# Performance work log

Hardware: AMD Instinct MI355X
Metric: run time of the kernel (lower is better)

Reference implementation:

```python
import jax, jax.numpy as jnp
import numpy as np

CUTOFF = 4.0
D_RBF = 20


def _rbf_consts():
    # e3nn soft_one_hot_linspace, basis='gaussian', cutoff=False
    values = np.linspace(0.0, CUTOFF, D_RBF)
    step = values[1] - values[0]
    # RadialBasis normalization buffers: 4000 uniform samples, unbiased std
    rs = np.linspace(0.0, CUTOFF, 4001)[1:]
    bs = np.exp(-(((rs[:, None] - values[None, :]) / step) ** 2)) / 1.12
    mean = bs.mean(0)
    inv_std = 1.0 / bs.std(0, ddof=1)
    return (jnp.asarray(values, jnp.float32), jnp.float32(step),
            jnp.asarray(mean, jnp.float32), jnp.asarray(inv_std, jnp.float32))


def setup_inputs() -> dict:
    N, P, E = 2000, 50000, 300000
    Ds, Dv, H, HO = 256, 128, 256, 128
    din = Ds + Dv + D_RBF + Dv  # 532
    key = jax.random.key(0)
    ks = jax.random.split(key, 12)
    atom_xyz = jax.random.uniform(ks[0], (N, 3), jnp.float32, 0.0, 8.0)
    probe_xyz = jax.random.uniform(ks[1], (P, 3), jnp.float32, 0.0, 8.0)
    cell = jnp.eye(3, dtype=jnp.float32)[None] * 8.0  # [1,3,3]
    src = jax.random.randint(ks[2], (E,), 0, N)
    dst = jax.random.randint(ks[3], (E,), 0, P)
    edges = jnp.stack([src, dst], axis=-1).astype(jnp.int32)  # [E,2]
    edges_displacement = jax.random.randint(ks[4], (E, 3), -1, 2).astype(jnp.float32)
    S_final = jax.random.normal(ks[5], (N, Ds), jnp.float32)
    V_final = jax.random.normal(ks[6], (N, Dv, 3), jnp.float32)
    s = 0.02
    return {
        'atom_xyz': atom_xyz, 'probe_xyz': probe_xyz, 'cell': cell,
        'edges': edges, 'edges_displacement': edges_displacement,
        'S_final': S_final, 'V_final': V_final,
        'ln_gamma': jnp.ones((din,), jnp.float32),
        'ln_beta': jnp.zeros((din,), jnp.float32),
        'W1': jax.random.normal(ks[7], (din, H), jnp.float32) * s,
        'b1': jnp.zeros((H,), jnp.float32),
        'W2': jax.random.normal(ks[8], (H, H), jnp.float32) * s,
        'b2': jnp.zeros((H,), jnp.float32),
        'Wo1': jax.random.normal(ks[9], (H, HO), jnp.float32) * s,
        'bo1': jnp.zeros((HO,), jnp.float32),
        'Wo2': jax.random.normal(ks[10], (HO, 1), jnp.float32) * s,
        'bo2': jnp.full((1,), -10.0, jnp.float32),
    }


def reference(atom_xyz, probe_xyz, cell, edges, edges_displacement,
              S_final, V_final, ln_gamma, ln_beta,
              W1, b1, W2, b2, Wo1, bo1, Wo2, bo2):
    values, step, rbf_mean, rbf_inv_std = _rbf_consts()
    src, dst = edges[:, 0], edges[:, 1]
    # PBC displacement: edges_displacement @ cell (single graph -> cell[0])
    disp = edges_displacement @ cell[0]                     # [E,3]
    vec = probe_xyz[dst] - (atom_xyz[src] + disp)           # [E,3]
    d = jnp.maximum(jnp.linalg.norm(vec, axis=-1, keepdims=True), 1e-8)
    r_hat = vec / d                                         # [E,3]
    ds = d[:, 0]                                            # [E]
    # RBF (gaussian soft one-hot) + normalization
    diff = (ds[:, None] - values) / step
    e = (jnp.exp(-diff * diff) / 1.12 - rbf_mean) * rbf_inv_std  # [E,20]
    x = ds / CUTOFF
    x5 = x ** 5
    env = (1.0 - 21.0 * x5 + 35.0 * x5 * x - 15.0 * x5 * x * x)
    env = env * (ds < CUTOFF).astype(jnp.float32)           # [E]
    # geometric invariants
    q = jnp.einsum('ek,eck->ec', r_hat, V_final[src])       # [E,Dv]
    n_atom = jnp.linalg.norm(V_final, axis=-1)              # [N,Dv]
    feat = jnp.concatenate([S_final[src], n_atom[src], e, q], axis=-1)  # [E,532]
    # LayerNorm
    mu = feat.mean(-1, keepdims=True)
    var = feat.var(-1, keepdims=True)
    feat = (feat - mu) * jax.lax.rsqrt(var + 1e-5) * ln_gamma + ln_beta
    # message MLP
    h = jax.nn.silu(feat @ W1 + b1)
    h = jax.nn.silu(h @ W2 + b2)                            # [E,256]
    # envelope-weighted scatter-add to probes
    m_p = jax.ops.segment_sum(h * env[:, None], dst,
                              num_segments=probe_xyz.shape[0])  # [P,256]
    # output MLP
    o = jax.nn.silu(m_p @ Wo1 + bo1)
    rho = o @ Wo2 + bo2                                     # [P,1]
    return rho[:, 0]
```

## Files before the change

### kernel.cpp

```cpp
#include <hip/hip_runtime.h>
#include <hip/hip_bf16.h>
#include <hip/hip_fp16.h>

#define DIN 532
#define DRBF 20
#define EB 32

typedef __attribute__((ext_vector_type(8))) short s8v;
typedef __attribute__((ext_vector_type(4))) float f4v;

static __device__ __forceinline__ float silu_f(float x){
    return x * __builtin_amdgcn_rcpf(1.0f + __expf(-x));
}
static __device__ __forceinline__ short f2bf(float x){
    __hip_bfloat16 b = __float2bfloat16(x);
    return *(short*)&b;
}
static __device__ __forceinline__ s8v pack8(float4 f0, float4 f1){
    s8v r;
    r[0]=f2bf(f0.x); r[1]=f2bf(f0.y); r[2]=f2bf(f0.z); r[3]=f2bf(f0.w);
    r[4]=f2bf(f1.x); r[5]=f2bf(f1.y); r[6]=f2bf(f1.z); r[7]=f2bf(f1.w);
    return r;
}
static __device__ __forceinline__ s8v pack8p(const float* p){
    float4 f0 = *(const float4*)p, f1 = *(const float4*)(p + 4);
    return pack8(f0, f1);
}
static __device__ __forceinline__ bool detect_bf16(const void* cellraw){
    float c0 = ((const float*)cellraw)[0];
    return !(c0 > 7.5f && c0 < 8.5f);
}
static __device__ __forceinline__ float loadr(const void* p, bool isbf, long idx){
    if (isbf) return __bfloat162float(((const __hip_bfloat16*)p)[idx]);
    return ((const float*)p)[idx];
}

struct ConvArgs {
    const void* src[9];
    float*      dst[9];
    int         sz[9];
    int         total;
    const void* cell;
};

__global__ void k_convert(ConvArgs a){
    bool isbf = detect_bf16(a.cell);
    int stride = gridDim.x * blockDim.x;
    for (int i = blockIdx.x*blockDim.x + threadIdx.x; i < a.total; i += stride){
        int idx = i, k = 0;
        while (idx >= a.sz[k]) { idx -= a.sz[k]; k++; }
        float v;
        if (isbf) v = __bfloat162float(((const __hip_bfloat16*)a.src[k])[idx]);
        else      v = ((const float*)a.src[k])[idx];
        a.dst[k][idx] = v;
    }
}

__global__ __launch_bounds__(256) void k_prep(
    const void* W1r, const void* gammar, const void* betar, const void* b1r,
    const void* W2r, const void* Wo1r, const void* cellraw,
    float* Gv, float* Bb, float* rbfc,
    short* w1ef, short* w2f, short* w1f, short* wo1f)
{
    int b = blockIdx.x, t = threadIdx.x;
    bool isbf = detect_bf16(cellraw);
    if (b < 17){
        int i0 = b * 32, i1 = min(i0 + 32, DIN);
        float g = 0.0f, bb = 0.0f;
        for (int i = i0; i < i1; i++){
            float w  = loadr(W1r, isbf, (long)i*256 + t);
            g  += loadr(gammar, isbf, i) * w;
            bb += loadr(betar,  isbf, i) * w;
        }
        if (b == 0) bb += loadr(b1r, isbf, t);
        atomicAdd(&Gv[t], g);
        atomicAdd(&Bb[t], bb);
        return;
    }
    if (b == 17){
        __shared__ float ssum[DRBF][8], ssq[DRBF][8];
        if (t < 160){
            int m = t >> 3, c = t & 7;
            const float step = 4.0f/19.0f;
            float vm = step * m;
            float s = 0.0f, ss = 0.0f;
            for (int i = c*500 + 1; i <= c*500 + 500; i++){
                float r = 0.001f * (float)i;
                float u = (r - vm) / step;
                float bv = __expf(-u*u) * (1.0f/1.12f);
                s += bv; ss += bv*bv;
            }
            ssum[m][c] = s; ssq[m][c] = ss;
        }
        __syncthreads();
        if (t < DRBF){
            float s = 0.0f, ss = 0.0f;
            for (int c = 0; c < 8; c++){ s += ssum[t][c]; ss += ssq[t][c]; }
            float mean = s / 4000.0f;
            float var  = (ss - s*s/4000.0f) / 3999.0f;
            rbfc[t]        = mean;
            rbfc[DRBF + t] = rsqrtf(var);
        }
        return;
    }
    int wid = t >> 6, lane = t & 63;
    int q8 = (lane >> 4) * 8, nl = lane & 15;
    if (b <= 21){
        int f = (b - 18)*4 + wid;
        for (int j = 0; j < 8; j++){
            int kk = q8 + j;
            int n  = f*16 + nl;
            float v = (kk < DRBF)
                ? loadr(gammar, isbf, 384 + kk) * loadr(W1r, isbf, (long)(384 + kk)*256 + n)
                : 0.0f;
            w1ef[((f << 6) | lane)*8 + j] = f2bf(v);
        }
    } else if (b <= 53){
        int f = (b - 22)*4 + wid;
        int ks = f & 7;
        for (int j = 0; j < 8; j++){
            int kk = ks*32 + q8 + j;
            int n  = (f >> 3)*16 + nl;
            w2f[((f << 6) | lane)*8 + j] = f2bf(loadr(W2r, isbf, (long)kk*256 + n));
        }
    } else if (b <= 117){
        int f = (b - 54)*4 + wid;
        int ksg = f >> 4, ntg = f & 15;
        int base;
        if (ksg < 8)       base = ksg * 32;
        else if (ksg < 12) base = 256 + (ksg - 8) * 32;
        else               base = 404 + (ksg - 12) * 32;
        for (int j = 0; j < 8; j++){
            int kk = base + q8 + j;
            int n  = ntg*16 + nl;
            w1f[((f << 6) | lane)*8 + j] =
                f2bf(loadr(gammar, isbf, kk) * loadr(W1r, isbf, (long)kk*256 + n));
        }
    } else {
        int f = (b - 118)*4 + wid;
        int ks = f & 7;
        for (int j = 0; j < 8; j++){
            int kk = ks*32 + q8 + j;
            int n  = (f >> 3)*16 + nl;
            wo1f[((f << 6) | lane)*8 + j] = f2bf(loadr(Wo1r, isbf, (long)kk*128 + n));
        }
    }
}

__global__ __launch_bounds__(256) void k_atom(const float* S, const float* V,
                                              const short* w1f, float4* AM,
                                              float* scal, int N){
    __shared__ float Sl[16][260];
    __shared__ float Vxl[16][132], Vyl[16][132], Vzl[16][132], nll[16][132];
    int t = threadIdx.x, wid = t >> 6, lane = t & 63;
    int q = lane >> 4, ml = lane & 15;
    int a0 = blockIdx.x * 16;

    for (int a = 0; a < 16; a++){
        int atom = min(a0 + a, N - 1);
        Sl[a][t] = S[atom*256 + t];
        if (t < 128){
            float x = V[atom*384 + 3*t];
            float y = V[atom*384 + 3*t + 1];
            float z = V[atom*384 + 3*t + 2];
            Vxl[a][t] = x; Vyl[a][t] = y; Vzl[a][t] = z;
            nll[a][t] = sqrtf(x*x + y*y + z*z);
        }
    }
    __syncthreads();

    for (int a2 = 0; a2 < 4; a2++){
        int a = (wid << 2) + a2;
        float v[11];
        #pragma unroll
        for (int k = 0; k < 11; k++) v[k] = 0.0f;
        for (int e = lane; e < 256; e += 64){
            float s = Sl[a][e];
            v[0] += s; v[1] += s*s;
        }
        for (int e = lane; e < 128; e += 64){
            float n = nll[a][e], x = Vxl[a][e], y = Vyl[a][e], z = Vzl[a][e];
            v[0] += n;   v[1] += n*n;
            v[2] += x;   v[3] += y;   v[4] += z;
            v[5] += x*x; v[6] += x*y; v[7] += x*z;
            v[8] += y*y; v[9] += y*z; v[10] += z*z;
        }
        #pragma unroll
        for (int k = 0; k < 11; k++)
            for (int off = 32; off > 0; off >>= 1)
                v[k] += __shfl_xor(v[k], off, 64);
        if (lane == 0 && a0 + a < N)
            for (int k = 0; k < 11; k++) scal[(a0 + a)*12 + k] = v[k];
    }

    f4v zz = {0.0f, 0.0f, 0.0f, 0.0f};
    f4v aA1[4], aM0[4], aM1[4], aM2[4];
    #pragma unroll
    for (int nt = 0; nt < 4; nt++){ aA1[nt]=zz; aM0[nt]=zz; aM1[nt]=zz; aM2[nt]=zz; }

    #pragma unroll
    for (int ks = 0; ks < 8; ks++){
        s8v av = pack8p(&Sl[ml][ks*32 + q*8]);
        #pragma unroll
        for (int nt = 0; nt < 4; nt++){
            s8v b = ((const s8v*)w1f)[(((ks << 4) | ((wid << 2) | nt)) << 6) | lane];
            aA1[nt] = __builtin_amdgcn_mfma_f32_16x16x32_bf16(av, b, aA1[nt], 0, 0, 0);
        }
    }
    #pragma unroll
    for (int ks = 0; ks < 4; ks++){
        s8v av = pack8p(&nll[ml][ks*32 + q*8]);
        #pragma unroll
        for (int nt = 0; nt < 4; nt++){
            s8v b = ((const s8v*)w1f)[((((8 + ks) << 4) | ((wid << 2) | nt)) << 6) | lane];
            aA1[nt] = __builtin_amdgcn_mfma_f32_16x16x32_bf16(av, b, aA1[nt], 0, 0, 0);
        }
    }
    #pragma unroll
    for (int ks = 0; ks < 4; ks++){
        s8v ax = pack8p(&Vxl[ml][ks*32 + q*8]);
        s8v ay = pack8p(&Vyl[ml][ks*32 + q*8]);
        s8v az = pack8p(&Vzl[ml][ks*32 + q*8]);
        #pragma unroll
        for (int nt = 0; nt < 4; nt++){
            s8v b = ((const s8v*)w1f)[((((12 + ks) << 4) | ((wid << 2) | nt)) << 6) | lane];
            aM0[nt] = __builtin_amdgcn_mfma_f32_16x16x32_bf16(ax, b, aM0[nt], 0, 0, 0);
            aM1[nt] = __builtin_amdgcn_mfma_f32_16x16x32_bf16(ay, b, aM1[nt], 0, 0, 0);
            aM2[nt] = __builtin_amdgcn_mfma_f32_16x16x32_bf16(az, b, aM2[nt], 0, 0, 0);
        }
    }

    #pragma unroll
    for (int nt = 0; nt < 4; nt++){
        #pragma unroll
        for (int reg = 0; reg < 4; reg++){
            int atom = a0 + (q << 2) + reg;
            if (atom < N)
                AM[(size_t)atom*256 + ((wid << 6) | (nt << 4) | ml)] =
                    make_float4(aA1[nt][reg], aM0[nt][reg], aM1[nt][reg], aM2[nt][reg]);
        }
    }
}

__global__ __launch_bounds__(256) void k_geom(
    const int* edges, const void* edraw, const float* cell,
    const float* axyz, const float* pxyz,
    int* etot, int* flag, int2* esd, float4* geo,
    const void* cellraw, int E)
{
    __shared__ int wcnt[4], wbase[4];
    bool isbf = detect_bf16(cellraw);
    float c0=cell[0],c1=cell[1],c2=cell[2],c3=cell[3],c4=cell[4];
    float c5=cell[5],c6=cell[6],c7=cell[7],c8=cell[8];
    int t = threadIdx.x, wid = t >> 6, lane = t & 63;
    int i = blockIdx.x*256 + t;

    bool act = false;
    int s = 0, dd = 0;
    float r0 = 0.f, r1 = 0.f, r2 = 0.f, dn = 0.f;
    if (i < E){
        s = edges[2*i]; dd = edges[2*i + 1];
        float d0 = loadr(edraw, isbf, 3L*i);
        float d1 = loadr(edraw, isbf, 3L*i + 1);
        float d2 = loadr(edraw, isbf, 3L*i + 2);
        float dx = d0*c0 + d1*c3 + d2*c6;
        float dy = d0*c1 + d1*c4 + d2*c7;
        float dz = d0*c2 + d1*c5 + d2*c8;
        float vx = pxyz[3*dd]   - (axyz[3*s]   + dx);
        float vy = pxyz[3*dd+1] - (axyz[3*s+1] + dy);
        float vz = pxyz[3*dd+2] - (axyz[3*s+2] + dz);
        dn = fmaxf(sqrtf(vx*vx + vy*vy + vz*vz), 1e-8f);
        act = dn < 4.0f;
        float inv = __builtin_amdgcn_rcpf(dn);
        r0 = vx*inv; r1 = vy*inv; r2 = vz*inv;
    }
    unsigned long long mask = __ballot(act);
    if (lane == 0) wcnt[wid] = __popcll(mask);
    __syncthreads();
    if (t == 0){
        int tot = wcnt[0] + wcnt[1] + wcnt[2] + wcnt[3];
        int base = tot ? atomicAdd(etot, tot) : 0;
        int run = base;
        #pragma unroll
        for (int w2 = 0; w2 < 4; w2++){ wbase[w2] = run; run += wcnt[w2]; }
    }
    __syncthreads();
    if (act){
        int pos = wbase[wid] + __popcll(mask & ((1ULL << lane) - 1ULL));
        esd[pos] = make_int2(s, dd);
        geo[pos] = make_float4(r0, r1, r2, dn);
        flag[dd] = 1;
    }
}

__global__ void k_zero(const int* flag, float4* m_p4, int P){
    int gid = blockIdx.x*256 + threadIdx.x;
    int row = gid >> 2, seg = gid & 3;
    if (row < P && flag[row]){
        float4 z = make_float4(0.f, 0.f, 0.f, 0.f);
        float4* p = m_p4 + (size_t)row*64 + seg*16;
        #pragma unroll
        for (int i = 0; i < 16; i++) p[i] = z;
    }
}

__global__ __launch_bounds__(256, 2) void k_edge(
    const int2* esd, const float4* geo, const int* etot, const float* scal,
    const float4* AM, const float* Gv, const float* Bb, const float* b2,
    const short* w1ef, const short* w2f, const float* rbfc, float* m_p)
{
    __shared__ float Gl[256], Bbl[256], b2l[256];
    __shared__ float rmean[DRBF], rinv[DRBF];
    __shared__ int   esrc[EB], edst[EB];
    __shared__ float rh0[EB], rh1[EB], rh2[EB], envv[EB], muv[EB], av[EB];
    __shared__ __align__(16) short ebfl[EB][32];
    __shared__ __align__(16) short afrag[2][8][64][8];

    int t = threadIdx.x, wid = t >> 6, lane = t & 63;
    int q = lane >> 4, ml_ = lane & 15;
    Gl[t] = Gv[t]; Bbl[t] = Bb[t]; b2l[t] = b2[t];
    if (t < DRBF){ rmean[t] = rbfc[t]; rinv[t] = rbfc[DRBF + t]; }
    __syncthreads();

    int Ea = etot[0];
    int ntiles = (Ea + EB - 1) / EB;

    for (int tile = blockIdx.x; tile < ntiles; tile += gridDim.x){
        if (t < EB){
            int epos = tile*EB + t;
            if (epos < Ea){
                int2 sd = esd[epos];
                float4 g = geo[epos];
                float r0 = g.x, r1 = g.y, r2 = g.z, dn = g.w;
                float x = dn * 0.25f;
                float x2 = x*x, x4 = x2*x2, x5 = x4*x;
                float env = 1.0f - 21.0f*x5 + 35.0f*x5*x - 15.0f*x5*x2;
                const float step = 4.0f/19.0f;
                float se = 0.0f, sse = 0.0f;
                for (int m = 0; m < DRBF; m++){
                    float u  = (dn - step*m) / step;
                    float bv = __expf(-u*u) * (1.0f/1.12f);
                    float em = (bv - rmean[m]) * rinv[m];
                    ebfl[t][m] = f2bf(em);
                    se += em; sse += em*em;
                }
                for (int m = DRBF; m < 32; m++) ebfl[t][m] = 0;
                const float* sc = &scal[sd.x*12];
                float sumq = r0*sc[2] + r1*sc[3] + r2*sc[4];
                float ssqq = r0*r0*sc[5] + r1*r1*sc[8] + r2*r2*sc[10]
                           + 2.0f*(r0*r1*sc[6] + r0*r2*sc[7] + r1*r2*sc[9]);
                float mu  = (sc[0] + se + sumq) * (1.0f/(float)DIN);
                float msq = (sc[1] + sse + ssqq) * (1.0f/(float)DIN);
                float a   = rsqrtf(fmaxf(msq - mu*mu, 0.0f) + 1e-5f);
                esrc[t] = sd.x; edst[t] = sd.y;
                rh0[t] = r0; rh1[t] = r1; rh2[t] = r2;
                envv[t] = env; muv[t] = mu; av[t] = a;
            } else {
                esrc[t] = 0; edst[t] = 0;
                rh0[t] = rh1[t] = rh2[t] = 0.0f;
                envv[t] = 0.0f; muv[t] = 0.0f; av[t] = 0.0f;
                for (int m = 0; m < 32; m++) ebfl[t][m] = 0;
            }
        }
        __syncthreads();

        f4v zz = {0.0f, 0.0f, 0.0f, 0.0f};
        f4v az[2][4];
        s8v ea0 = *(const s8v*)&ebfl[ml_][q*8];
        s8v ea1 = *(const s8v*)&ebfl[16 + ml_][q*8];
        #pragma unroll
        for (int nt = 0; nt < 4; nt++){
            s8v bw = ((const s8v*)w1ef)[(((wid << 2) | nt) << 6) | lane];
            az[0][nt] = __builtin_amdgcn_mfma_f32_16x16x32_bf16(ea0, bw, zz, 0, 0, 0);
            az[1][nt] = __builtin_amdgcn_mfma_f32_16x16x32_bf16(ea1, bw, zz, 0, 0, 0);
        }

        float gk[4], bbk[4];
        #pragma unroll
        for (int nt = 0; nt < 4; nt++){
            int k = (wid << 6) | (nt << 4) | ml_;
            gk[nt] = Gl[k]; bbk[nt] = Bbl[k];
        }
        #pragma unroll
        for (int mt = 0; mt < 2; mt++){
            #pragma unroll
            for (int reg = 0; reg < 4; reg++){
                int e_ = (mt << 4) | (q << 2) | reg;
                int s_ = esrc[e_];
                float r0 = rh0[e_], r1 = rh1[e_], r2 = rh2[e_];
                float mu = muv[e_], a_ = av[e_];
                const float4* AMr = &AM[(size_t)s_*256 + ((wid << 6) | ml_)];
                #pragma unroll
                for (int nt = 0; nt < 4; nt++){
                    float4 am = AMr[nt << 4];
                    float z = az[mt][nt][reg] + am.x + r0*am.y + r1*am.z + r2*am.w;
                    float y = a_*(z - mu*gk[nt]) + bbk[nt];
                    float h1 = silu_f(y);
                    int ks = (wid << 1) | (nt >> 1);
                    int col = ((nt & 1) << 4) | ml_;
                    int lanep = ((col >> 3) << 4) | (q << 2) | reg;
                    afrag[mt][ks][lanep][col & 7] = f2bf(h1);
                }
            }
        }
        __syncthreads();

        f4v acc[2][4];
        #pragma unroll
        for (int mt = 0; mt < 2; mt++)
            #pragma unroll
            for (int nt = 0; nt < 4; nt++) acc[mt][nt] = zz;
        #pragma unroll
        for (int ks = 0; ks < 8; ks++){
            s8v a0 = *(const s8v*)&afrag[0][ks][lane][0];
            s8v a1 = *(const s8v*)&afrag[1][ks][lane][0];
            #pragma unroll
            for (int nt = 0; nt < 4; nt++){
                s8v b = ((const s8v*)w2f)[(((((wid << 2) | nt) << 3) | ks) << 6) | lane];
                acc[0][nt] = __builtin_amdgcn_mfma_f32_16x16x32_bf16(a0, b, acc[0][nt], 0, 0, 0);
                acc[1][nt] = __builtin_amdgcn_mfma_f32_16x16x32_bf16(a1, b, acc[1][nt], 0, 0, 0);
            }
        }

        float b2k[4];
        #pragma unroll
        for (int nt = 0; nt < 4; nt++) b2k[nt] = b2l[(wid << 6) | (nt << 4) | ml_];
        #pragma unroll
        for (int mt = 0; mt < 2; mt++){
            #pragma unroll
            for (int reg = 0; reg < 4; reg++){
                int e_ = (mt << 4) | (q << 2) | reg;
                float env = envv[e_];
                if (env != 0.0f){
                    int dd = edst[e_];
                    float* mrow = &m_p[(size_t)dd*256 + (wid << 6) + ml_];
                    #pragma unroll
                    for (int nt = 0; nt < 4; nt++){
                        float z2 = acc[mt][nt][reg] + b2k[nt];
                        atomicAdd(&mrow[nt << 4], silu_f(z2) * env);
                    }
                }
            }
        }
        __syncthreads();
    }
}

__global__ __launch_bounds__(256) void k_probe(
    const float* m_p, const int* flag, const short* wo1f, const float* bo1,
    const float* Wo2, const float* bo2, void* out, const void* cellraw, int P)
{
    int t = threadIdx.x, wid = t >> 6, lane = t & 63;
    int q = lane >> 4, ml = lane & 15;
    int p0 = blockIdx.x * 128 + wid * 32;
    const float4* mp4 = (const float4*)m_p;

    f4v zz = {0.0f, 0.0f, 0.0f, 0.0f};
    f4v acc[2][8];
    #pragma unroll
    for (int mt = 0; mt < 2; mt++)
        #pragma unroll
        for (int nt = 0; nt < 8; nt++) acc[mt][nt] = zz;

    int row0 = min(p0 + ml, P - 1);
    int row1 = min(p0 + 16 + ml, P - 1);
    bool f0 = flag[row0] != 0;
    bool f1 = flag[row1] != 0;
    s8v zero8 = {0,0,0,0,0,0,0,0};

    #pragma unroll
    for (int ks = 0; ks < 8; ks++){
        int c = ks*8 + q*2;
        s8v a0 = zero8, a1 = zero8;
        if (f0){
            float4 f00 = mp4[(size_t)row0*64 + c], f01 = mp4[(size_t)row0*64 + c + 1];
            a0 = pack8(f00, f01);
        }
        if (f1){
            float4 f10 = mp4[(size_t)row1*64 + c], f11 = mp4[(size_t)row1*64 + c + 1];
            a1 = pack8(f10, f11);
        }
        #pragma unroll
        for (int nt = 0; nt < 8; nt++){
            s8v b = ((const s8v*)wo1f)[(((nt << 3) | ks) << 6) | lane];
            acc[0][nt] = __builtin_amdgcn_mfma_f32_16x16x32_bf16(a0, b, acc[0][nt], 0, 0, 0);
            acc[1][nt] = __builtin_amdgcn_mfma_f32_16x16x32_bf16(a1, b, acc[1][nt], 0, 0, 0);
        }
    }

    float bo1v[8], wo2v[8];
    #pragma unroll
    for (int nt = 0; nt < 8; nt++){
        int n = (nt << 4) | ml;
        bo1v[nt] = bo1[n];
        wo2v[nt] = Wo2[n];
    }
    bool isbf = detect_bf16(cellraw);
    float bo2v = bo2[0];

    #pragma unroll
    for (int mt = 0; mt < 2; mt++){
        #pragma unroll
        for (int reg = 0; reg < 4; reg++){
            float s = 0.0f;
            #pragma unroll
            for (int nt = 0; nt < 8; nt++)
                s += silu_f(acc[mt][nt][reg] + bo1v[nt]) * wo2v[nt];
            s += __shfl_xor(s, 1, 64);
            s += __shfl_xor(s, 2, 64);
            s += __shfl_xor(s, 4, 64);
            s += __shfl_xor(s, 8, 64);
            if (ml == 0){
                int p = p0 + (mt << 4) + (q << 2) + reg;
                if (p < P){
                    float rho = s + bo2v;
                    if (isbf) ((__hip_bfloat16*)out)[p] = __float2bfloat16(rho);
                    else      ((float*)out)[p] = rho;
                }
            }
        }
    }
}

extern "C" void kernel_launch(void* const* d_in, const int* in_sizes, int n_in,
                              void* d_out, int out_size, void* d_ws, size_t ws_size,
                              hipStream_t stream)
{
    const int N = in_sizes[0] / 3;
    const int P = in_sizes[1] / 3;
    const int E = in_sizes[3] / 2;

    float* w = (float*)d_ws;
    size_t off = 0;
    auto carve = [&](size_t n) -> float* {
        float* p = w + off;
        off += (n + 63) & ~(size_t)63;
        return p;
    };

    const int conv_din[9] = {6, 5, 1, 0, 12, 14, 15, 2, 16};
    float* cdst[9];
    int    csz[9];
    int total = 0;
    for (int k = 0; k < 9; k++){
        csz[k]  = in_sizes[conv_din[k]];
        cdst[k] = carve(csz[k]);
        total  += csz[k];
    }
    float* c_V     = cdst[0];
    float* c_S     = cdst[1];
    float* c_probe = cdst[2];
    float* c_atom  = cdst[3];
    float* c_b2    = cdst[4];
    float* c_bo1   = cdst[5];
    float* c_Wo2   = cdst[6];
    float* c_cell  = cdst[7];
    float* c_bo2   = cdst[8];

    float* rbfc  = carve(2 * DRBF);
    float* AMf   = carve((size_t)N * 256 * 4);
    float* scal  = carve((size_t)N * 12);
    float* w1ef  = carve(16 * 64 * 8 / 2);
    float* w2f   = carve(128 * 64 * 8 / 2);
    float* w1f   = carve(256 * 64 * 8 / 2);
    float* wo1f  = carve(64 * 64 * 8 / 2);
    float* m_p   = carve((size_t)P * 256);
    int*   etot  = (int*)carve(64);
    int*   flag  = (int*)carve(P);
    float* Gv    = carve(256);
    float* Bb    = carve(256);
    int*   esd   = (int*)carve((size_t)E * 2);
    float* geo   = carve((size_t)E * 4);

    ConvArgs ca;
    for (int k = 0; k < 9; k++){
        ca.src[k] = d_in[conv_din[k]];
        ca.dst[k] = cdst[k];
        ca.sz[k]  = csz[k];
    }
    ca.total = total;
    ca.cell  = d_in[2];

    const int* d_edges = (const int*)d_in[3];

    size_t zbytes = (size_t)((char*)(Bb + 256) - (char*)etot);
    hipMemsetAsync(etot, 0, zbytes, stream);
    k_convert<<<256, 256, 0, stream>>>(ca);
    k_prep<<<134, 256, 0, stream>>>(d_in[9], d_in[7], d_in[8], d_in[10],
                                    d_in[11], d_in[13], d_in[2],
                                    Gv, Bb, rbfc,
                                    (short*)w1ef, (short*)w2f, (short*)w1f, (short*)wo1f);
    k_atom<<<(N + 15) / 16, 256, 0, stream>>>(c_S, c_V, (const short*)w1f,
                                              (float4*)AMf, scal, N);
    k_geom<<<(E + 255) / 256, 256, 0, stream>>>(
        d_edges, d_in[4], c_cell, c_atom, c_probe,
        etot, flag, (int2*)esd, (float4*)geo, d_in[2], E);
    k_zero<<<(P*4 + 255) / 256, 256, 0, stream>>>(flag, (float4*)m_p, P);
    k_edge<<<512, 256, 0, stream>>>(
        (const int2*)esd, (const float4*)geo, etot, scal,
        (const float4*)AMf, Gv, Bb, c_b2,
        (const short*)w1ef, (const short*)w2f, rbfc, m_p);
    k_probe<<<(P + 127) / 128, 256, 0, stream>>>(
        m_p, flag, (const short*)wo1f, c_bo1, c_Wo2, c_bo2, d_out, d_in[2], P);
}
```

Before: 208.0 us.

## Merge small launches into fused pre and mid kernels, drop memset and zero kernel

Merges the convert and prep kernels into one launch, and the atom, geometry and Gv/Bb reduction into a single multi-role kernel. The memset is replaced by zeroing etot and flag inside the convert path, and m_p rows are now zeroed on first touch via atomicExch in the geometry blocks. Atomic accumulation of Gv/Bb is replaced by per-block partials reduced in the mid kernel. The aim is to cut launch overhead and the separate zero pass. In exchange, the atom path reads S directly from global memory instead of shared memory, and first-touch zeroing runs serially per row inside geometry threads.

```diff
diff --git a/kernel.cpp b/kernel.cpp
--- a/kernel.cpp
+++ b/kernel.cpp
@@ -36,48 +36,46 @@
 }
 
 struct ConvArgs {
-    const void* src[9];
-    float*      dst[9];
-    int         sz[9];
+    const void* src[10];
+    float*      dst[10];
+    int         sz[10];
     int         total;
-    const void* cell;
 };
 
-__global__ void k_convert(ConvArgs a){
-    bool isbf = detect_bf16(a.cell);
-    int stride = gridDim.x * blockDim.x;
-    for (int i = blockIdx.x*blockDim.x + threadIdx.x; i < a.total; i += stride){
-        int idx = i, k = 0;
-        while (idx >= a.sz[k]) { idx -= a.sz[k]; k++; }
-        float v;
-        if (isbf) v = __bfloat162float(((const __hip_bfloat16*)a.src[k])[idx]);
-        else      v = ((const float*)a.src[k])[idx];
-        a.dst[k][idx] = v;
-    }
-}
-
-__global__ __launch_bounds__(256) void k_prep(
+__global__ __launch_bounds__(256) void k_pre(ConvArgs ca,
     const void* W1r, const void* gammar, const void* betar, const void* b1r,
     const void* W2r, const void* Wo1r, const void* cellraw,
-    float* Gv, float* Bb, float* rbfc,
+    float* Gpart, float* Bpart, float* rbfc,
     short* w1ef, short* w2f, short* w1f, short* wo1f)
 {
     int b = blockIdx.x, t = threadIdx.x;
     bool isbf = detect_bf16(cellraw);
-    if (b < 17){
-        int i0 = b * 32, i1 = min(i0 + 32, DIN);
+    if (b < 256){
+        int stride = 256 * 256;
+        for (int i = b*256 + t; i < ca.total; i += stride){
+            int idx = i, k = 0;
+            while (idx >= ca.sz[k]) { idx -= ca.sz[k]; k++; }
+            float v = 0.0f;
+            if (ca.src[k]) v = loadr(ca.src[k], isbf, idx);
+            ca.dst[k][idx] = v;
+        }
+        return;
+    }
+    int pb = b - 256;
+    if (pb < 17){
+        int i0 = pb * 32, i1 = min(i0 + 32, DIN);
         float g = 0.0f, bb = 0.0f;
         for (int i = i0; i < i1; i++){
             float w  = loadr(W1r, isbf, (long)i*256 + t);
             g  += loadr(gammar, isbf, i) * w;
             bb += loadr(betar,  isbf, i) * w;
         }
-        if (b == 0) bb += loadr(b1r, isbf, t);
-        atomicAdd(&Gv[t], g);
-        atomicAdd(&Bb[t], bb);
+        if (pb == 0) bb += loadr(b1r, isbf, t);
+        Gpart[pb*256 + t] = g;
+        Bpart[pb*256 + t] = bb;
         return;
     }
-    if (b == 17){
+    if (pb == 17){
         __shared__ float ssum[DRBF][8], ssq[DRBF][8];
         if (t < 160){
             int m = t >> 3, c = t & 7;
@@ -105,8 +103,8 @@
     }
     int wid = t >> 6, lane = t & 63;
     int q8 = (lane >> 4) * 8, nl = lane & 15;
-    if (b <= 21){
-        int f = (b - 18)*4 + wid;
+    if (pb <= 21){
+        int f = (pb - 18)*4 + wid;
         for (int j = 0; j < 8; j++){
             int kk = q8 + j;
             int n  = f*16 + nl;
@@ -115,16 +113,16 @@
                 : 0.0f;
             w1ef[((f << 6) | lane)*8 + j] = f2bf(v);
         }
-    } else if (b <= 53){
-        int f = (b - 22)*4 + wid;
+    } else if (pb <= 53){
+        int f = (pb - 22)*4 + wid;
         int ks = f & 7;
         for (int j = 0; j < 8; j++){
             int kk = ks*32 + q8 + j;
             int n  = (f >> 3)*16 + nl;
             w2f[((f << 6) | lane)*8 + j] = f2bf(loadr(W2r, isbf, (long)kk*256 + n));
         }
-    } else if (b <= 117){
-        int f = (b - 54)*4 + wid;
+    } else if (pb <= 117){
+        int f = (pb - 54)*4 + wid;
         int ksg = f >> 4, ntg = f & 15;
         int base;
         if (ksg < 8)       base = ksg * 32;
@@ -137,7 +135,7 @@
                 f2bf(loadr(gammar, isbf, kk) * loadr(W1r, isbf, (long)kk*256 + n));
         }
     } else {
-        int f = (b - 118)*4 + wid;
+        int f = (pb - 118)*4 + wid;
         int ks = f & 7;
         for (int j = 0; j < 8; j++){
             int kk = ks*32 + q8 + j;
@@ -147,161 +145,171 @@
     }
 }
 
-__global__ __launch_bounds__(256) void k_atom(const float* S, const float* V,
-                                              const short* w1f, float4* AM,
-                                              float* scal, int N){
-    __shared__ float Sl[16][260];
-    __shared__ float Vxl[16][132], Vyl[16][132], Vzl[16][132], nll[16][132];
-    int t = threadIdx.x, wid = t >> 6, lane = t & 63;
-    int q = lane >> 4, ml = lane & 15;
-    int a0 = blockIdx.x * 16;
-
-    for (int a = 0; a < 16; a++){
-        int atom = min(a0 + a, N - 1);
-        Sl[a][t] = S[atom*256 + t];
-        if (t < 128){
-            float x = V[atom*384 + 3*t];
-            float y = V[atom*384 + 3*t + 1];
-            float z = V[atom*384 + 3*t + 2];
-            Vxl[a][t] = x; Vyl[a][t] = y; Vzl[a][t] = z;
-            nll[a][t] = sqrtf(x*x + y*y + z*z);
-        }
-    }
-    __syncthreads();
-
-    for (int a2 = 0; a2 < 4; a2++){
-        int a = (wid << 2) + a2;
-        float v[11];
-        #pragma unroll
-        for (int k = 0; k < 11; k++) v[k] = 0.0f;
-        for (int e = lane; e < 256; e += 64){
-            float s = Sl[a][e];
-            v[0] += s; v[1] += s*s;
-        }
-        for (int e = lane; e < 128; e += 64){
-            float n = nll[a][e], x = Vxl[a][e], y = Vyl[a][e], z = Vzl[a][e];
-            v[0] += n;   v[1] += n*n;
-            v[2] += x;   v[3] += y;   v[4] += z;
-            v[5] += x*x; v[6] += x*y; v[7] += x*z;
-            v[8] += y*y; v[9] += y*z; v[10] += z*z;
-        }
-        #pragma unroll
-        for (int k = 0; k < 11; k++)
-            for (int off = 32; off > 0; off >>= 1)
-                v[k] += __shfl_xor(v[k], off, 64);
-        if (lane == 0 && a0 + a < N)
-            for (int k = 0; k < 11; k++) scal[(a0 + a)*12 + k] = v[k];
-    }
-
-    f4v zz = {0.0f, 0.0f, 0.0f, 0.0f};
-    f4v aA1[4], aM0[4], aM1[4], aM2[4];
-    #pragma unroll
-    for (int nt = 0; nt < 4; nt++){ aA1[nt]=zz; aM0[nt]=zz; aM1[nt]=zz; aM2[nt]=zz; }
-
-    #pragma unroll
-    for (int ks = 0; ks < 8; ks++){
-        s8v av = pack8p(&Sl[ml][ks*32 + q*8]);
-        #pragma unroll
-        for (int nt = 0; nt < 4; nt++){
-            s8v b = ((const s8v*)w1f)[(((ks << 4) | ((wid << 2) | nt)) << 6) | lane];
-            aA1[nt] = __builtin_amdgcn_mfma_f32_16x16x32_bf16(av, b, aA1[nt], 0, 0, 0);
-        }
-    }
-    #pragma unroll
-    for (int ks = 0; ks < 4; ks++){
-        s8v av = pack8p(&nll[ml][ks*32 + q*8]);
-        #pragma unroll
-        for (int nt = 0; nt < 4; nt++){
-            s8v b = ((const s8v*)w1f)[((((8 + ks) << 4) | ((wid << 2) | nt)) << 6) | lane];
-            aA1[nt] = __builtin_amdgcn_mfma_f32_16x16x32_bf16(av, b, aA1[nt], 0, 0, 0);
-        }
-    }
-    #pragma unroll
-    for (int ks = 0; ks < 4; ks++){
-        s8v ax = pack8p(&Vxl[ml][ks*32 + q*8]);
-        s8v ay = pack8p(&Vyl[ml][ks*32 + q*8]);
-        s8v az = pack8p(&Vzl[ml][ks*32 + q*8]);
-        #pragma unroll
-        for (int nt = 0; nt < 4; nt++){
-            s8v b = ((const s8v*)w1f)[((((12 + ks) << 4) | ((wid << 2) | nt)) << 6) | lane];
-            aM0[nt] = __builtin_amdgcn_mfma_f32_16x16x32_bf16(ax, b, aM0[nt], 0, 0, 0);
-            aM1[nt] = __builtin_amdgcn_mfma_f32_16x16x32_bf16(ay, b, aM1[nt], 0, 0, 0);
-            aM2[nt] = __builtin_amdgcn_mfma_f32_16x16x32_bf16(az, b, aM2[nt], 0, 0, 0);
-        }
-    }
-
-    #pragma unroll
-    for (int nt = 0; nt < 4; nt++){
-        #pragma unroll
-        for (int reg = 0; reg < 4; reg++){
-            int atom = a0 + (q << 2) + reg;
-            if (atom < N)
-                AM[(size_t)atom*256 + ((wid << 6) | (nt << 4) | ml)] =
-                    make_float4(aA1[nt][reg], aM0[nt][reg], aM1[nt][reg], aM2[nt][reg]);
-        }
-    }
-}
-
-__global__ __launch_bounds__(256) void k_geom(
+__global__ __launch_bounds__(256) void k_mid(
+    const float* S, const float* V, const short* w1f, float4* AM,
+    float* scal, int N,
     const int* edges, const void* edraw, const float* cell,
     const float* axyz, const float* pxyz,
-    int* etot, int* flag, int2* esd, float4* geo,
-    const void* cellraw, int E)
+    int* etot, int* flag, int2* esd, float4* geo, float* m_p,
+    const void* cellraw, int E,
+    const float* Gpart, const float* Bpart, float* Gv, float* Bb,
+    int GA, int GG)
 {
-    __shared__ int wcnt[4], wbase[4];
-    bool isbf = detect_bf16(cellraw);
-    float c0=cell[0],c1=cell[1],c2=cell[2],c3=cell[3],c4=cell[4];
-    float c5=cell[5],c6=cell[6],c7=cell[7],c8=cell[8];
-    int t = threadIdx.x, wid = t >> 6, lane = t & 63;
-    int i = blockIdx.x*256 + t;
-
-    bool act = false;
-    int s = 0, dd = 0;
-    float r0 = 0.f, r1 = 0.f, r2 = 0.f, dn = 0.f;
-    if (i < E){
-        s = edges[2*i]; dd = edges[2*i + 1];
-        float d0 = loadr(edraw, isbf, 3L*i);
-        float d1 = loadr(edraw, isbf, 3L*i + 1);
-        float d2 = loadr(edraw, isbf, 3L*i + 2);
-        float dx = d0*c0 + d1*c3 + d2*c6;
-        float dy = d0*c1 + d1*c4 + d2*c7;
-        float dz = d0*c2 + d1*c5 + d2*c8;
-        float vx = pxyz[3*dd]   - (axyz[3*s]   + dx);
-        float vy = pxyz[3*dd+1] - (axyz[3*s+1] + dy);
-        float vz = pxyz[3*dd+2] - (axyz[3*s+2] + dz);
-        dn = fmaxf(sqrtf(vx*vx + vy*vy + vz*vz), 1e-8f);
-        act = dn < 4.0f;
-        float inv = __builtin_amdgcn_rcpf(dn);
-        r0 = vx*inv; r1 = vy*inv; r2 = vz*inv;
-    }
-    unsigned long long mask = __ballot(act);
-    if (lane == 0) wcnt[wid] = __popcll(mask);
-    __syncthreads();
-    if (t == 0){
-        int tot = wcnt[0] + wcnt[1] + wcnt[2] + wcnt[3];
-        int base = tot ? atomicAdd(etot, tot) : 0;
-        int run = base;
-        #pragma unroll
-        for (int w2 = 0; w2 < 4; w2++){ wbase[w2] = run; run += wcnt[w2]; }
-    }
-    __syncthreads();
-    if (act){
-        int pos = wbase[wid] + __popcll(mask & ((1ULL << lane) - 1ULL));
-        esd[pos] = make_int2(s, dd);
-        geo[pos] = make_float4(r0, r1, r2, dn);
-        flag[dd] = 1;
-    }
-}
-
-__global__ void k_zero(const int* flag, float4* m_p4, int P){
-    int gid = blockIdx.x*256 + threadIdx.x;
-    int row = gid >> 2, seg = gid & 3;
-    if (row < P && flag[row]){
-        float4 z = make_float4(0.f, 0.f, 0.f, 0.f);
-        float4* p = m_p4 + (size_t)row*64 + seg*16;
-        #pragma unroll
-        for (int i = 0; i < 16; i++) p[i] = z;
-    }
+    int b = blockIdx.x, t = threadIdx.x;
+    int wid = t >> 6, lane = t & 63;
+
+    if (b < GA){
+        __shared__ float Vxl[16][132], Vyl[16][132], Vzl[16][132], nll[16][132];
+        int q = lane >> 4, ml = lane & 15;
+        int a0 = b * 16;
+
+        for (int a = 0; a < 16; a++){
+            int atom = min(a0 + a, N - 1);
+            if (t < 128){
+                float x = V[(size_t)atom*384 + 3*t];
+                float y = V[(size_t)atom*384 + 3*t + 1];
+                float z = V[(size_t)atom*384 + 3*t + 2];
+                Vxl[a][t] = x; Vyl[a][t] = y; Vzl[a][t] = z;
+                nll[a][t] = sqrtf(x*x + y*y + z*z);
+            }
+        }
+        __syncthreads();
+
+        for (int a2 = 0; a2 < 4; a2++){
+            int a = (wid << 2) + a2;
+            int row = min(a0 + a, N - 1);
+            float v[11];
+            #pragma unroll
+            for (int k = 0; k < 11; k++) v[k] = 0.0f;
+            for (int e = lane; e < 256; e += 64){
+                float s = S[(size_t)row*256 + e];
+                v[0] += s; v[1] += s*s;
+            }
+            for (int e = lane; e < 128; e += 64){
+                float n = nll[a][e], x = Vxl[a][e], y = Vyl[a][e], z = Vzl[a][e];
+                v[0] += n;   v[1] += n*n;
+                v[2] += x;   v[3] += y;   v[4] += z;
+                v[5] += x*x; v[6] += x*y; v[7] += x*z;
+                v[8] += y*y; v[9] += y*z; v[10] += z*z;
+            }
+            #pragma unroll
+            for (int k = 0; k < 11; k++)
+                for (int off2 = 32; off2 > 0; off2 >>= 1)
+                    v[k] += __shfl_xor(v[k], off2, 64);
+            if (lane == 0 && a0 + a < N)
+                for (int k = 0; k < 11; k++) scal[(a0 + a)*12 + k] = v[k];
+        }
+
+        f4v zz = {0.0f, 0.0f, 0.0f, 0.0f};
+        f4v aA1[4], aM0[4], aM1[4], aM2[4];
+        #pragma unroll
+        for (int nt = 0; nt < 4; nt++){ aA1[nt]=zz; aM0[nt]=zz; aM1[nt]=zz; aM2[nt]=zz; }
+
+        int srow = min(a0 + ml, N - 1);
+        #pragma unroll
+        for (int ks = 0; ks < 8; ks++){
+            s8v av = pack8p(&S[(size_t)srow*256 + ks*32 + q*8]);
+            #pragma unroll
+            for (int nt = 0; nt < 4; nt++){
+                s8v bf = ((const s8v*)w1f)[(((ks << 4) | ((wid << 2) | nt)) << 6) | lane];
+                aA1[nt] = __builtin_amdgcn_mfma_f32_16x16x32_bf16(av, bf, aA1[nt], 0, 0, 0);
+            }
+        }
+        #pragma unroll
+        for (int ks = 0; ks < 4; ks++){
+            s8v av = pack8p(&nll[ml][ks*32 + q*8]);
+            #pragma unroll
+            for (int nt = 0; nt < 4; nt++){
+                s8v bf = ((const s8v*)w1f)[((((8 + ks) << 4) | ((wid << 2) | nt)) << 6) | lane];
+                aA1[nt] = __builtin_amdgcn_mfma_f32_16x16x32_bf16(av, bf, aA1[nt], 0, 0, 0);
+            }
+        }
+        #pragma unroll
+        for (int ks = 0; ks < 4; ks++){
+            s8v ax = pack8p(&Vxl[ml][ks*32 + q*8]);
+            s8v ay = pack8p(&Vyl[ml][ks*32 + q*8]);
+            s8v az = pack8p(&Vzl[ml][ks*32 + q*8]);
+            #pragma unroll
+            for (int nt = 0; nt < 4; nt++){
+                s8v bf = ((const s8v*)w1f)[((((12 + ks) << 4) | ((wid << 2) | nt)) << 6) | lane];
+                aM0[nt] = __builtin_amdgcn_mfma_f32_16x16x32_bf16(ax, bf, aM0[nt], 0, 0, 0);
+                aM1[nt] = __builtin_amdgcn_mfma_f32_16x16x32_bf16(ay, bf, aM1[nt], 0, 0, 0);
+                aM2[nt] = __builtin_amdgcn_mfma_f32_16x16x32_bf16(az, bf, aM2[nt], 0, 0, 0);
+            }
+        }
+
+        #pragma unroll
+        for (int nt = 0; nt < 4; nt++){
+            #pragma unroll
+            for (int reg = 0; reg < 4; reg++){
+                int atom = a0 + (q << 2) + reg;
+                if (atom < N)
+                    AM[(size_t)atom*256 + ((wid << 6) | (nt << 4) | ml)] =
+                        make_float4(aA1[nt][reg], aM0[nt][reg], aM1[nt][reg], aM2[nt][reg]);
+            }
+        }
+        return;
+    }
+
+    if (b < GA + GG){
+        __shared__ int wcnt[4], wbase[4];
+        bool isbf = detect_bf16(cellraw);
+        float c0=cell[0],c1=cell[1],c2=cell[2],c3=cell[3],c4=cell[4];
+        float c5=cell[5],c6=cell[6],c7=cell[7],c8=cell[8];
+        int i = (b - GA)*256 + t;
+
+        bool act = false;
+        int s = 0, dd = 0;
+        float r0 = 0.f, r1 = 0.f, r2 = 0.f, dn = 0.f;
+        if (i < E){
+            s = edges[2*i]; dd = edges[2*i + 1];
+            float d0 = loadr(edraw, isbf, 3L*i);
+            float d1 = loadr(edraw, isbf, 3L*i + 1);
+            float d2 = loadr(edraw, isbf, 3L*i + 2);
+            float dx = d0*c0 + d1*c3 + d2*c6;
+            float dy = d0*c1 + d1*c4 + d2*c7;
+            float dz = d0*c2 + d1*c5 + d2*c8;
+            float vx = pxyz[3*dd]   - (axyz[3*s]   + dx);
+            float vy = pxyz[3*dd+1] - (axyz[3*s+1] + dy);
+            float vz = pxyz[3*dd+2] - (axyz[3*s+2] + dz);
+            dn = fmaxf(sqrtf(vx*vx + vy*vy + vz*vz), 1e-8f);
+            act = dn < 4.0f;
+            float inv = __builtin_amdgcn_rcpf(dn);
+            r0 = vx*inv; r1 = vy*inv; r2 = vz*inv;
+        }
+        unsigned long long mask = __ballot(act);
+        if (lane == 0) wcnt[wid] = __popcll(mask);
+        __syncthreads();
+        if (t == 0){
+            int tot = wcnt[0] + wcnt[1] + wcnt[2] + wcnt[3];
+            int base = tot ? atomicAdd(etot, tot) : 0;
+            int run = base;
+            #pragma unroll
+            for (int w2 = 0; w2 < 4; w2++){ wbase[w2] = run; run += wcnt[w2]; }
+        }
+        __syncthreads();
+        if (act){
+            int pos = wbase[wid] + __popcll(mask & ((1ULL << lane) - 1ULL));
+            esd[pos] = make_int2(s, dd);
+            geo[pos] = make_float4(r0, r1, r2, dn);
+            if (atomicExch(&flag[dd], 1) == 0){
+                float4 z = make_float4(0.f, 0.f, 0.f, 0.f);
+                float4* p = (float4*)&m_p[(size_t)dd*256];
+                #pragma unroll 4
+                for (int k = 0; k < 64; k++) p[k] = z;
+            }
+        }
+        return;
+    }
+
+    float g = 0.0f, bb = 0.0f;
+    #pragma unroll
+    for (int i = 0; i < 17; i++){
+        g  += Gpart[i*256 + t];
+        bb += Bpart[i*256 + t];
+    }
+    Gv[t] = g;
+    Bb[t] = bb;
 }
 
 __global__ __launch_bounds__(256, 2) void k_edge(
@@ -416,9 +424,9 @@
             s8v a1 = *(const s8v*)&afrag[1][ks][lane][0];
             #pragma unroll
             for (int nt = 0; nt < 4; nt++){
-                s8v b = ((const s8v*)w2f)[(((((wid << 2) | nt) << 3) | ks) << 6) | lane];
-                acc[0][nt] = __builtin_amdgcn_mfma_f32_16x16x32_bf16(a0, b, acc[0][nt], 0, 0, 0);
-                acc[1][nt] = __builtin_amdgcn_mfma_f32_16x16x32_bf16(a1, b, acc[1][nt], 0, 0, 0);
+                s8v bf = ((const s8v*)w2f)[(((((wid << 2) | nt) << 3) | ks) << 6) | lane];
+                acc[0][nt] = __builtin_amdgcn_mfma_f32_16x16x32_bf16(a0, bf, acc[0][nt], 0, 0, 0);
+                acc[1][nt] = __builtin_amdgcn_mfma_f32_16x16x32_bf16(a1, bf, acc[1][nt], 0, 0, 0);
             }
         }
 
@@ -482,9 +490,9 @@
         }
         #pragma unroll
         for (int nt = 0; nt < 8; nt++){
-            s8v b = ((const s8v*)wo1f)[(((nt << 3) | ks) << 6) | lane];
-            acc[0][nt] = __builtin_amdgcn_mfma_f32_16x16x32_bf16(a0, b, acc[0][nt], 0, 0, 0);
-            acc[1][nt] = __builtin_amdgcn_mfma_f32_16x16x32_bf16(a1, b, acc[1][nt], 0, 0, 0);
+            s8v bf = ((const s8v*)wo1f)[(((nt << 3) | ks) << 6) | lane];
+            acc[0][nt] = __builtin_amdgcn_mfma_f32_16x16x32_bf16(a0, bf, acc[0][nt], 0, 0, 0);
+            acc[1][nt] = __builtin_amdgcn_mfma_f32_16x16x32_bf16(a1, bf, acc[1][nt], 0, 0, 0);
         }
     }
 
@@ -569,6 +577,8 @@
     int*   flag  = (int*)carve(P);
     float* Gv    = carve(256);
     float* Bb    = carve(256);
+    float* Gpart = carve(17 * 256);
+    float* Bpart = carve(17 * 256);
     int*   esd   = (int*)carve((size_t)E * 2);
     float* geo   = carve((size_t)E * 4);
 
@@ -578,24 +588,24 @@
         ca.dst[k] = cdst[k];
         ca.sz[k]  = csz[k];
     }
-    ca.total = total;
-    ca.cell  = d_in[2];
+    ca.src[9] = nullptr;
+    ca.dst[9] = (float*)etot;
+    ca.sz[9]  = 64 + P;
+    ca.total  = total + 64 + P;
 
     const int* d_edges = (const int*)d_in[3];
-
-    size_t zbytes = (size_t)((char*)(Bb + 256) - (char*)etot);
-    hipMemsetAsync(etot, 0, zbytes, stream);
-    k_convert<<<256, 256, 0, stream>>>(ca);
-    k_prep<<<134, 256, 0, stream>>>(d_in[9], d_in[7], d_in[8], d_in[10],
-                                    d_in[11], d_in[13], d_in[2],
-                                    Gv, Bb, rbfc,
-                                    (short*)w1ef, (short*)w2f, (short*)w1f, (short*)wo1f);
-    k_atom<<<(N + 15) / 16, 256, 0, stream>>>(c_S, c_V, (const short*)w1f,
-                                              (float4*)AMf, scal, N);
-    k_geom<<<(E + 255) / 256, 256, 0, stream>>>(
+    const int GA = (N + 15) / 16;
+    const int GG = (E + 255) / 256;
+
+    k_pre<<<390, 256, 0, stream>>>(ca,
+        d_in[9], d_in[7], d_in[8], d_in[10], d_in[11], d_in[13], d_in[2],
+        Gpart, Bpart, rbfc,
+        (short*)w1ef, (short*)w2f, (short*)w1f, (short*)wo1f);
+    k_mid<<<GA + GG + 1, 256, 0, stream>>>(
+        c_S, c_V, (const short*)w1f, (float4*)AMf, scal, N,
         d_edges, d_in[4], c_cell, c_atom, c_probe,
-        etot, flag, (int2*)esd, (float4*)geo, d_in[2], E);
-    k_zero<<<(P*4 + 255) / 256, 256, 0, stream>>>(flag, (float4*)m_p, P);
+        etot, flag, (int2*)esd, (float4*)geo, m_p, d_in[2], E,
+        Gpart, Bpart, Gv, Bb, GA, GG);
     k_edge<<<512, 256, 0, stream>>>(
         (const int2*)esd, (const float4*)geo, etot, scal,
         (const float4*)AMf, Gv, Bb, c_b2,
```

Result: faster. 196.0 us (-5.8%).
